# Kernel optimization log

Measured on AMD Instinct MI355X. Metric: run time of the kernel, lower is better.

Reference implementation:

```python
import jax, jax.numpy as jnp
import numpy as np

N_NODES = 50000
N_EDGES = 800000
NUM_MOL = 2000
MSG_PASSES = 4


def setup_inputs() -> dict:
    key = jax.random.key(0)
    ks = jax.random.split(key, 16)
    x = jax.random.randint(ks[0], (N_NODES,), 0, 119)
    edge_attr = jax.random.randint(ks[1], (N_EDGES,), 0, 4)
    edge_index = jax.random.randint(ks[2], (2, N_EDGES), 0, N_NODES)
    batch = jnp.sort(jax.random.randint(ks[3], (N_NODES,), 0, NUM_MOL))
    f32 = jnp.float32
    return {
        "x": x,
        "edge_attr": edge_attr,
        "edge_index": edge_index,
        "batch": batch,
        "atom_table": jax.random.normal(ks[4], (119, 128), f32) * 0.1,
        "bond_table": jax.random.normal(ks[5], (4, 64), f32) * 0.1,
        "Wi": jax.random.normal(ks[6], (192, 128), f32) * 0.05,
        "bi": jax.random.normal(ks[7], (128,), f32) * 0.01,
        "Wu1": jax.random.normal(ks[8], (320, 128), f32) * 0.05,
        "bu1": jax.random.normal(ks[9], (128,), f32) * 0.01,
        "Wu2": jax.random.normal(ks[10], (128, 128), f32) * 0.05,
        "bu2": jax.random.normal(ks[11], (128,), f32) * 0.01,
        "Wr1": jax.random.normal(ks[12], (128, 512), f32) * 0.05,
        "br1": jax.random.normal(ks[13], (512,), f32) * 0.01,
        "Wr2": jax.random.normal(ks[14], (512, 1), f32) * 0.05,
        "br2": jax.random.normal(ks[15], (1,), f32) * 0.01,
    }


def reference(x, edge_attr, edge_index, batch,
              atom_table, bond_table, Wi, bi, Wu1, bu1, Wu2, bu2,
              Wr1, br1, Wr2, br2):
    atom = atom_table[x]                      # [N, atom_emb]
    bond = bond_table[edge_attr]              # [E, bond_emb]
    src, dst = edge_index[0], edge_index[1]
    a_src = atom[src]                         # [E, atom_emb]
    ab = jnp.concatenate([a_src, bond], axis=1)  # [E, atom_emb+bond_emb]
    msg = jax.nn.relu(ab @ Wi + bi)           # [E, msg_dim]
    for _ in range(MSG_PASSES):
        agg = jax.ops.segment_sum(msg, dst, num_segments=N_NODES)  # [N, msg_dim]
        upd_in = jnp.concatenate([ab, agg[src]], axis=1)           # [E, 320]
        h = jax.nn.relu(upd_in @ Wu1 + bu1)
        msg = jax.nn.relu(h @ Wu2 + bu2)
    node_state = jax.ops.segment_sum(msg, dst, num_segments=N_NODES)
    mol_state = jax.ops.segment_sum(node_state, batch, num_segments=NUM_MOL)
    out = jax.nn.relu(mol_state @ Wr1 + br1) @ Wr2 + br2  # [NUM_MOL, 1]
    return jnp.squeeze(out, axis=-1)
```

## Files before the change

kernel.cpp:

```cpp
#include <hip/hip_runtime.h>
#include <hip/hip_bf16.h>

#define N_NODES 50000
#define N_EDGES 800000
#define NUM_MOL 2000

typedef __attribute__((ext_vector_type(8))) short short8;
typedef __attribute__((ext_vector_type(4))) float f32x4;

union bfbits { __hip_bfloat16 b; short s; };

__global__ void k_tables(const float* __restrict__ atom_table,
                         const float* __restrict__ bond_table,
                         const float* __restrict__ Wi,
                         const float* __restrict__ bi,
                         const float* __restrict__ Wu1,
                         const float* __restrict__ bu1,
                         float* __restrict__ T1, float* __restrict__ U1,
                         float* __restrict__ T2c, float* __restrict__ U2c) {
  int b = blockIdx.x;
  int c = threadIdx.x;
  if (b < 119) {
    float t = 0.f, u = 0.f;
    for (int k = 0; k < 128; k++) {
      float a = atom_table[b * 128 + k];
      t += a * Wi[k * 128 + c];
      u += a * Wu1[k * 128 + c];
    }
    T1[b * 128 + c] = t;
    U1[b * 128 + c] = u;
  } else {
    int a = b - 119;
    float t = bi[c], u = bu1[c];
    for (int k = 0; k < 64; k++) {
      float bv = bond_table[a * 64 + k];
      t += bv * Wi[(128 + k) * 128 + c];
      u += bv * Wu1[(128 + k) * 128 + c];
    }
    T2c[a * 128 + c] = t;
    U2c[a * 128 + c] = u;
  }
}

__global__ void k_prep(const float* __restrict__ T1, const float* __restrict__ T2c,
                       const float* __restrict__ Wu2, const float* __restrict__ Wu1,
                       float* __restrict__ TT,
                       short* __restrict__ Wt, short* __restrict__ Wlo,
                       short* __restrict__ W1t, short* __restrict__ W1lo) {
  int b = blockIdx.x;
  int k = threadIdx.x;
  if (b < 476) {
    float v = T1[(b >> 2) * 128 + k] + T2c[(b & 3) * 128 + k];
    TT[b * 128 + k] = v > 0.f ? v : 0.f;
  } else if (b < 604) {
    int n = b - 476;
    float w = Wu2[k * 128 + n];
    bfbits hi; hi.b = __float2bfloat16(w);
    float hf = __bfloat162float(hi.b);
    bfbits lo; lo.b = __float2bfloat16(w - hf);
    Wt[n * 128 + k] = hi.s;
    Wlo[n * 128 + k] = lo.s;
  } else {
    int n = b - 604;
    float w = Wu1[(192 + k) * 128 + n];
    bfbits hi; hi.b = __float2bfloat16(w);
    float hf = __bfloat162float(hi.b);
    bfbits lo; lo.b = __float2bfloat16(w - hf);
    W1t[n * 128 + k] = hi.s;
    W1lo[n * 128 + k] = lo.s;
  }
}

__global__ void k_fillb(const int* __restrict__ eidx, const int* __restrict__ attr,
                        const int* __restrict__ x,
                        int* __restrict__ cnt, int* __restrict__ csr1) {
  int e = blockIdx.x * 256 + threadIdx.x;
  int d = eidx[N_EDGES + e];
  int s = eidx[e];
  int a = attr[e];
  int pos = atomicAdd(&cnt[d], 1);
  if (pos < 64) {
    int packed = (s * 4 + a) | ((x[s] * 4 + a) << 18);
    csr1[d * 64 + pos] = packed;
  }
}

__global__ void k_molptr(const int* __restrict__ batch, int* __restrict__ molptr) {
  int m = blockIdx.x * 256 + threadIdx.x;
  if (m > NUM_MOL) return;
  int lo = 0, hi = N_NODES;
  while (lo < hi) {
    int mid = (lo + hi) >> 1;
    if (batch[mid] < m) lo = mid + 1; else hi = mid;
  }
  molptr[m] = lo;
}

__global__ void k_gather0(const int* __restrict__ cnt, const int* __restrict__ csr1,
                          const float* __restrict__ TT, float* __restrict__ A_) {
  int n = blockIdx.x * 4 + (threadIdx.x >> 6);
  int lane = threadIdx.x & 63;
  int g = lane >> 5;
  int p = lane & 31;
  int beg = n * 64;
  int end = beg + cnt[n];
  float s0 = 0.f, s1 = 0.f, s2 = 0.f, s3 = 0.f;
  int i = beg;
  for (; i + 7 < end; i += 8) {
    int iA = ((unsigned)csr1[i + g]) >> 18;
    int iB = ((unsigned)csr1[i + 2 + g]) >> 18;
    int iC = ((unsigned)csr1[i + 4 + g]) >> 18;
    int iD = ((unsigned)csr1[i + 6 + g]) >> 18;
    float4 va = *(const float4*)&TT[iA * 128 + p * 4];
    float4 vb = *(const float4*)&TT[iB * 128 + p * 4];
    float4 vc = *(const float4*)&TT[iC * 128 + p * 4];
    float4 vd = *(const float4*)&TT[iD * 128 + p * 4];
    s0 += (va.x + vb.x) + (vc.x + vd.x);
    s1 += (va.y + vb.y) + (vc.y + vd.y);
    s2 += (va.z + vb.z) + (vc.z + vd.z);
    s3 += (va.w + vb.w) + (vc.w + vd.w);
  }
  for (; i + 3 < end; i += 4) {
    int iA = ((unsigned)csr1[i + g]) >> 18;
    int iB = ((unsigned)csr1[i + 2 + g]) >> 18;
    float4 va = *(const float4*)&TT[iA * 128 + p * 4];
    float4 vb = *(const float4*)&TT[iB * 128 + p * 4];
    s0 += va.x + vb.x; s1 += va.y + vb.y;
    s2 += va.z + vb.z; s3 += va.w + vb.w;
  }
  for (; i < end; i += 2) {
    if (i + g < end) {
      int idx = ((unsigned)csr1[i + g]) >> 18;
      float4 v = *(const float4*)&TT[idx * 128 + p * 4];
      s0 += v.x; s1 += v.y; s2 += v.z; s3 += v.w;
    }
  }
  s0 += __shfl_xor(s0, 32, 64);
  s1 += __shfl_xor(s1, 32, 64);
  s2 += __shfl_xor(s2, 32, 64);
  s3 += __shfl_xor(s3, 32, 64);
  float2 o;
  o.x = (g == 0) ? s0 : s2;
  o.y = (g == 0) ? s1 : s3;
  *(float2*)&A_[n * 128 + p * 4 + g * 2] = o;
}

__global__ void k_gather(const int* __restrict__ cnt, const int* __restrict__ csr1,
                         const __hip_bfloat16* __restrict__ M, float* __restrict__ A_) {
  int n = blockIdx.x * 4 + (threadIdx.x >> 6);
  int lane = threadIdx.x & 63;
  int g = lane >> 4;
  int p = lane & 15;
  int beg = n * 64;
  int end = beg + cnt[n];
  float s[8];
#pragma unroll
  for (int j = 0; j < 8; j++) s[j] = 0.f;
  const short* Ms = (const short*)M;
  int i = beg;
  for (; i + 15 < end; i += 16) {
    int iA = csr1[i + g] & 0x3FFFF;
    int iB = csr1[i + 4 + g] & 0x3FFFF;
    int iC = csr1[i + 8 + g] & 0x3FFFF;
    int iD = csr1[i + 12 + g] & 0x3FFFF;
    short8 va = *(const short8*)&Ms[iA * 128 + p * 8];
    short8 vb = *(const short8*)&Ms[iB * 128 + p * 8];
    short8 vc = *(const short8*)&Ms[iC * 128 + p * 8];
    short8 vd = *(const short8*)&Ms[iD * 128 + p * 8];
#pragma unroll
    for (int j = 0; j < 4; j++) {
      float2 fa = __bfloat1622float2(*(const __hip_bfloat162*)&((const short*)&va)[j * 2]);
      float2 fb = __bfloat1622float2(*(const __hip_bfloat162*)&((const short*)&vb)[j * 2]);
      float2 fc = __bfloat1622float2(*(const __hip_bfloat162*)&((const short*)&vc)[j * 2]);
      float2 fd = __bfloat1622float2(*(const __hip_bfloat162*)&((const short*)&vd)[j * 2]);
      s[j * 2] += (fa.x + fb.x) + (fc.x + fd.x);
      s[j * 2 + 1] += (fa.y + fb.y) + (fc.y + fd.y);
    }
  }
  for (; i + 7 < end; i += 8) {
    int iA = csr1[i + g] & 0x3FFFF;
    int iB = csr1[i + 4 + g] & 0x3FFFF;
    short8 va = *(const short8*)&Ms[iA * 128 + p * 8];
    short8 vb = *(const short8*)&Ms[iB * 128 + p * 8];
#pragma unroll
    for (int j = 0; j < 4; j++) {
      float2 fa = __bfloat1622float2(*(const __hip_bfloat162*)&((const short*)&va)[j * 2]);
      float2 fb = __bfloat1622float2(*(const __hip_bfloat162*)&((const short*)&vb)[j * 2]);
      s[j * 2] += fa.x + fb.x;
      s[j * 2 + 1] += fa.y + fb.y;
    }
  }
  for (; i < end; i += 4) {
    if (i + g < end) {
      int idx = csr1[i + g] & 0x3FFFF;
      short8 va = *(const short8*)&Ms[idx * 128 + p * 8];
#pragma unroll
      for (int j = 0; j < 4; j++) {
        float2 fa = __bfloat1622float2(*(const __hip_bfloat162*)&((const short*)&va)[j * 2]);
        s[j * 2] += fa.x;
        s[j * 2 + 1] += fa.y;
      }
    }
  }
#pragma unroll
  for (int j = 0; j < 8; j++) s[j] += __shfl_xor(s[j], 16, 64);
#pragma unroll
  for (int j = 0; j < 8; j++) s[j] += __shfl_xor(s[j], 32, 64);
  float2 o;
  o.x = s[g * 2];
  o.y = s[g * 2 + 1];
  *(float2*)&A_[n * 128 + p * 8 + g * 2] = o;
}

__global__ __launch_bounds__(256, 2) void k_mm1m(const float* __restrict__ A_,
                                                 const short* __restrict__ W1t,
                                                 const short* __restrict__ W1lo,
                                                 const int* __restrict__ x,
                                                 const float* __restrict__ U1,
                                                 float* __restrict__ B2_) {
  __shared__ short wh[8192];
  __shared__ short wl[8192];
  __shared__ float mbuf[4][16][68];
  int t = threadIdx.x;
  int lane = t & 63;
  int m = lane & 15;
  int quad = lane >> 4;
  int wslot = t >> 6;
  int h = blockIdx.x & 1;

  for (int idx = t; idx < 1024; idx += 256) {
    int nl = idx >> 4;
    int c16 = idx & 15;
    int off = nl * 256 + c16 * 16;
    int so = (off ^ ((nl & 7) << 4)) >> 1;
    *(short8*)&wh[so] = *(const short8*)((const char*)W1t + (h * 64 + nl) * 256 + c16 * 16);
    *(short8*)&wl[so] = *(const short8*)((const char*)W1lo + (h * 64 + nl) * 256 + c16 * 16);
  }
  int nb[4], nx[4];
#pragma unroll
  for (int nt = 0; nt < 4; nt++) {
    int nl = nt * 16 + m;
    nb[nt] = nl * 256;
    nx[nt] = (nl & 7) << 4;
  }
  __syncthreads();

  for (int s = (blockIdx.x >> 1) * 4 + wslot; s < 3125; s += 2048) {
    int row = s * 16 + m;
    f32x4 acc[4];
#pragma unroll
    for (int nt = 0; nt < 4; nt++) acc[nt] = (f32x4){0.f, 0.f, 0.f, 0.f};

#pragma unroll
    for (int kc = 0; kc < 4; kc++) {
      int k0 = kc * 32 + quad * 8;
      short8 ahi, alo;
      {
        float av[8];
        *(float4*)&av[0] = *(const float4*)&A_[row * 128 + k0];
        *(float4*)&av[4] = *(const float4*)&A_[row * 128 + k0 + 4];
#pragma unroll
        for (int j = 0; j < 8; j++) {
          float hv = av[j];
          bfbits hi; hi.b = __float2bfloat16(hv);
          float hf = __bfloat162float(hi.b);
          bfbits lo; lo.b = __float2bfloat16(hv - hf);
          ahi[j] = hi.s;
          alo[j] = lo.s;
        }
      }
      int kb = k0 * 2;
#pragma unroll
      for (int nt = 0; nt < 4; nt++) {
        int so = ((nb[nt] + kb) ^ nx[nt]) >> 1;
        short8 whv = *(const short8*)&wh[so];
        short8 wlv = *(const short8*)&wl[so];
        acc[nt] = __builtin_amdgcn_mfma_f32_16x16x32_bf16(ahi, whv, acc[nt], 0, 0, 0);
        acc[nt] = __builtin_amdgcn_mfma_f32_16x16x32_bf16(alo, whv, acc[nt], 0, 0, 0);
        acc[nt] = __builtin_amdgcn_mfma_f32_16x16x32_bf16(ahi, wlv, acc[nt], 0, 0, 0);
      }
    }

#pragma unroll
    for (int nt = 0; nt < 4; nt++)
#pragma unroll
      for (int r = 0; r < 4; r++)
        mbuf[wslot][quad * 4 + r][nt * 16 + m] = acc[nt][r];
#pragma unroll
    for (int p = 0; p < 4; p++) {
      int c = p * 64 + lane;
      int rr = c >> 4;
      int qf = c & 15;
      int n = s * 16 + rr;
      int xn = x[n];
      float4 v = *(const float4*)&mbuf[wslot][rr][qf * 4];
      float4 d = *(const float4*)&U1[xn * 128 + h * 64 + qf * 4];
      v.x += d.x; v.y += d.y; v.z += d.z; v.w += d.w;
      *(float4*)&B2_[n * 128 + h * 64 + qf * 4] = v;
    }
  }
}

__global__ __launch_bounds__(256, 2) void k_mm2(const float* __restrict__ B2_,
                                                const float* __restrict__ U2c,
                                                const short* __restrict__ Wt,
                                                const short* __restrict__ Wlo,
                                                const float* __restrict__ bu2,
                                                __hip_bfloat16* __restrict__ M) {
  __shared__ short wh[16384];
  __shared__ short wl[16384];
  __shared__ short mbuf[4][16][68];
  int t = threadIdx.x;
  int lane = t & 63;
  int m = lane & 15;
  int quad = lane >> 4;
  int wslot = t >> 6;
  int w0 = blockIdx.x * 4 + wslot;
  int h = w0 & 1;

  for (int idx = t; idx < 2048; idx += 256) {
    int n = idx >> 4;
    int c16 = idx & 15;
    int off = n * 256 + c16 * 16;
    int so = (off ^ ((n & 7) << 4)) >> 1;
    *(short8*)&wh[so] = *(const short8*)((const char*)Wt + off);
    *(short8*)&wl[so] = *(const short8*)((const char*)Wlo + off);
  }
  float bias[4];
  int nb[4], nx[4];
#pragma unroll
  for (int nt = 0; nt < 4; nt++) {
    int n = h * 64 + nt * 16 + m;
    bias[nt] = bu2[n];
    nb[nt] = n * 256;
    nx[nt] = (n & 7) << 4;
  }
  __syncthreads();

  for (int tid = w0; tid < 25000; tid += 4096) {
    int s = tid >> 1;
    int node = s * 4 + (m >> 2);
    int attr = m & 3;
    f32x4 acc[4];
#pragma unroll
    for (int nt = 0; nt < 4; nt++) acc[nt] = (f32x4){0.f, 0.f, 0.f, 0.f};

#pragma unroll
    for (int kc = 0; kc < 4; kc++) {
      int k0 = kc * 32 + quad * 8;
      short8 ahi, alo;
      {
        float bba[8], u2a[8];
        *(float4*)&bba[0] = *(const float4*)&B2_[node * 128 + k0];
        *(float4*)&bba[4] = *(const float4*)&B2_[node * 128 + k0 + 4];
        *(float4*)&u2a[0] = *(const float4*)&U2c[attr * 128 + k0];
        *(float4*)&u2a[4] = *(const float4*)&U2c[attr * 128 + k0 + 4];
#pragma unroll
        for (int j = 0; j < 8; j++) {
          float hv = bba[j] + u2a[j];
          hv = hv > 0.f ? hv : 0.f;
          bfbits hi; hi.b = __float2bfloat16(hv);
          float hf = __bfloat162float(hi.b);
          bfbits lo; lo.b = __float2bfloat16(hv - hf);
          ahi[j] = hi.s;
          alo[j] = lo.s;
        }
      }
      int kb = k0 * 2;
#pragma unroll
      for (int nt = 0; nt < 4; nt++) {
        int so = ((nb[nt] + kb) ^ nx[nt]) >> 1;
        short8 whv = *(const short8*)&wh[so];
        short8 wlv = *(const short8*)&wl[so];
        acc[nt] = __builtin_amdgcn_mfma_f32_16x16x32_bf16(ahi, whv, acc[nt], 0, 0, 0);
        acc[nt] = __builtin_amdgcn_mfma_f32_16x16x32_bf16(alo, whv, acc[nt], 0, 0, 0);
        acc[nt] = __builtin_amdgcn_mfma_f32_16x16x32_bf16(ahi, wlv, acc[nt], 0, 0, 0);
      }
    }

#pragma unroll
    for (int nt = 0; nt < 4; nt++) {
#pragma unroll
      for (int r = 0; r < 4; r++) {
        float v = acc[nt][r] + bias[nt];
        v = v > 0.f ? v : 0.f;
        bfbits o; o.b = __float2bfloat16(v);
        mbuf[wslot][quad * 4 + r][nt * 16 + m] = o.s;
      }
    }
    {
      int rr = lane >> 2;
      int qq = lane & 3;
      short8 v = *(const short8*)&mbuf[wslot][rr][qq * 8];
      *(short8*)((short*)M + (s * 16 + rr) * 128 + h * 64 + qq * 8) = v;
      short8 v2 = *(const short8*)&mbuf[wslot][rr][(qq + 4) * 8];
      *(short8*)((short*)M + (s * 16 + rr) * 128 + h * 64 + (qq + 4) * 8) = v2;
    }
  }
}

__global__ void k_molgather(const float* __restrict__ A_, const int* __restrict__ molptr,
                            float* __restrict__ mol) {
  int m = blockIdx.x * 4 + (threadIdx.x >> 6);
  int lane = threadIdx.x & 63;
  int beg = molptr[m], end = molptr[m + 1];
  float ax = 0.f, ay = 0.f;
  int n = beg;
  for (; n + 1 < end; n += 2) {
    float2 v0 = *(const float2*)&A_[n * 128 + lane * 2];
    float2 v1 = *(const float2*)&A_[(n + 1) * 128 + lane * 2];
    ax += v0.x + v1.x;
    ay += v0.y + v1.y;
  }
  if (n < end) {
    float2 v0 = *(const float2*)&A_[n * 128 + lane * 2];
    ax += v0.x;
    ay += v0.y;
  }
  float2 o; o.x = ax; o.y = ay;
  *(float2*)&mol[m * 128 + lane * 2] = o;
}

__global__ __launch_bounds__(256) void k_readout(const float* __restrict__ mol,
                                                 const float* __restrict__ Wr1,
                                                 const float* __restrict__ br1,
                                                 const float* __restrict__ Wr2,
                                                 const float* __restrict__ br2,
                                                 float* __restrict__ out) {
  int m0 = blockIdx.x * 8;
  __shared__ float ms[8][128];
  __shared__ float red[32];
  int t = threadIdx.x;
  int lane = t & 63;
  int wave = t >> 6;
  for (int i = t; i < 1024; i += 256)
    ms[i >> 7][i & 127] = mol[m0 * 128 + i];
  __syncthreads();
  float part[8];
#pragma unroll
  for (int q = 0; q < 8; q++) part[q] = 0.f;
#pragma unroll
  for (int jj = 0; jj < 2; jj++) {
    int j = t + jj * 256;
    float b1 = br1[j];
    float acc[8];
#pragma unroll
    for (int q = 0; q < 8; q++) acc[q] = b1;
    for (int k = 0; k < 128; k += 4) {
      float w0 = Wr1[k * 512 + j];
      float w1 = Wr1[(k + 1) * 512 + j];
      float w2 = Wr1[(k + 2) * 512 + j];
      float w3 = Wr1[(k + 3) * 512 + j];
#pragma unroll
      for (int q = 0; q < 8; q++)
        acc[q] += ms[q][k] * w0 + ms[q][k + 1] * w1 + ms[q][k + 2] * w2 + ms[q][k + 3] * w3;
    }
    float w2v = Wr2[j];
#pragma unroll
    for (int q = 0; q < 8; q++) {
      float a = acc[q] > 0.f ? acc[q] : 0.f;
      part[q] += a * w2v;
    }
  }
#pragma unroll
  for (int q = 0; q < 8; q++) {
    float v = part[q];
    v += __shfl_xor(v, 32, 64);
    v += __shfl_xor(v, 16, 64);
    v += __shfl_xor(v, 8, 64);
    v += __shfl_xor(v, 4, 64);
    v += __shfl_xor(v, 2, 64);
    v += __shfl_xor(v, 1, 64);
    if (lane == 0) red[wave * 8 + q] = v;
  }
  __syncthreads();
  if (t < 8)
    out[m0 + t] = red[t] + red[8 + t] + red[16 + t] + red[24 + t] + br2[0];
}

extern "C" void kernel_launch(void* const* d_in, const int* in_sizes, int n_in,
                              void* d_out, int out_size, void* d_ws, size_t ws_size,
                              hipStream_t stream) {
  const int* x        = (const int*)d_in[0];
  const int* eattr    = (const int*)d_in[1];
  const int* eidx     = (const int*)d_in[2];
  const int* batch    = (const int*)d_in[3];
  const float* atom_table = (const float*)d_in[4];
  const float* bond_table = (const float*)d_in[5];
  const float* Wi  = (const float*)d_in[6];
  const float* bi  = (const float*)d_in[7];
  const float* Wu1 = (const float*)d_in[8];
  const float* bu1 = (const float*)d_in[9];
  const float* Wu2 = (const float*)d_in[10];
  const float* bu2 = (const float*)d_in[11];
  const float* Wr1 = (const float*)d_in[12];
  const float* br1 = (const float*)d_in[13];
  const float* Wr2 = (const float*)d_in[14];
  const float* br2 = (const float*)d_in[15];
  float* out = (float*)d_out;

  char* ws = (char*)d_ws;
  __hip_bfloat16* M = (__hip_bfloat16*)(ws);
  short* Wt      = (short*)(ws + 51200000);
  short* Wlo     = (short*)(ws + 51232768);
  short* W1t     = (short*)(ws + 51265536);
  short* W1lo    = (short*)(ws + 51298304);
  int*   molptr  = (int*)  (ws + 51331072);
  int*   cnt     = (int*)  (ws + 51340000);
  int*   csr1    = (int*)  (ws + 52000000);
  float* A       = (float*)(ws + 102400000);
  float* B2      = (float*)(ws + 128000000);
  float* T1      = (float*)(ws + 157000064);
  float* U1      = (float*)(ws + 157060992);
  float* T2c     = (float*)(ws + 157121920);
  float* U2c     = (float*)(ws + 157123968);
  float* TT      = (float*)(ws + 157126016);
  float* mol     = (float*)(ws + 157369728);

  hipMemsetAsync(cnt, 0, N_NODES * sizeof(int), stream);
  k_tables<<<123, 128, 0, stream>>>(atom_table, bond_table, Wi, bi, Wu1, bu1,
                                    T1, U1, T2c, U2c);
  k_prep<<<732, 128, 0, stream>>>(T1, T2c, Wu2, Wu1, TT, Wt, Wlo, W1t, W1lo);
  k_fillb<<<N_EDGES / 256, 256, 0, stream>>>(eidx, eattr, x, cnt, csr1);
  k_molptr<<<(NUM_MOL + 256) / 256, 256, 0, stream>>>(batch, molptr);

  k_gather0<<<N_NODES / 4, 256, 0, stream>>>(cnt, csr1, TT, A);

  for (int p = 0; p < 4; p++) {
    k_mm1m<<<1024, 256, 0, stream>>>(A, W1t, W1lo, x, U1, B2);
    k_mm2<<<1024, 256, 0, stream>>>(B2, U2c, Wt, Wlo, bu2, M);
    k_gather<<<N_NODES / 4, 256, 0, stream>>>(cnt, csr1, M, A);
  }

  k_molgather<<<NUM_MOL / 4, 256, 0, stream>>>(A, molptr, mol);
  k_readout<<<NUM_MOL / 8, 256, 0, stream>>>(mol, Wr1, br1, Wr2, br2, out);
}
```

Baseline: 547.1 us.

## Restructure k_mm2 so each block holds one weight half and loops over bond attrs

Each block now loads only its half of the second-layer weights into shared memory, which halves LDS per block. Each wave processes 16 nodes and loops over all 4 bond attributes, reusing one B2 row load across four (node, attr) rows instead of reloading per attribute. The output row mapping changes to (node*4+attr). This quadruples the accumulator registers (16 f32x4 per lane), which may reduce occupancy.

After: 767.0 us. 1.4x slower.

```diff
diff --git a/kernel.cpp b/kernel.cpp
--- a/kernel.cpp
+++ b/kernel.cpp
@@ -307,54 +307,56 @@
                                                 const short* __restrict__ Wlo,
                                                 const float* __restrict__ bu2,
                                                 __hip_bfloat16* __restrict__ M) {
-  __shared__ short wh[16384];
-  __shared__ short wl[16384];
+  __shared__ short wh[8192];
+  __shared__ short wl[8192];
   __shared__ short mbuf[4][16][68];
   int t = threadIdx.x;
   int lane = t & 63;
   int m = lane & 15;
   int quad = lane >> 4;
   int wslot = t >> 6;
-  int w0 = blockIdx.x * 4 + wslot;
-  int h = w0 & 1;
-
-  for (int idx = t; idx < 2048; idx += 256) {
-    int n = idx >> 4;
+  int h = blockIdx.x & 1;
+
+  for (int idx = t; idx < 1024; idx += 256) {
+    int nl = idx >> 4;
     int c16 = idx & 15;
-    int off = n * 256 + c16 * 16;
-    int so = (off ^ ((n & 7) << 4)) >> 1;
-    *(short8*)&wh[so] = *(const short8*)((const char*)Wt + off);
-    *(short8*)&wl[so] = *(const short8*)((const char*)Wlo + off);
+    int off = nl * 256 + c16 * 16;
+    int so = (off ^ ((nl & 7) << 4)) >> 1;
+    *(short8*)&wh[so] = *(const short8*)((const char*)Wt + (h * 64 + nl) * 256 + c16 * 16);
+    *(short8*)&wl[so] = *(const short8*)((const char*)Wlo + (h * 64 + nl) * 256 + c16 * 16);
   }
   float bias[4];
   int nb[4], nx[4];
 #pragma unroll
   for (int nt = 0; nt < 4; nt++) {
-    int n = h * 64 + nt * 16 + m;
-    bias[nt] = bu2[n];
-    nb[nt] = n * 256;
-    nx[nt] = (n & 7) << 4;
+    int nl = nt * 16 + m;
+    bias[nt] = bu2[h * 64 + nl];
+    nb[nt] = nl * 256;
+    nx[nt] = (nl & 7) << 4;
   }
   __syncthreads();
 
-  for (int tid = w0; tid < 25000; tid += 4096) {
-    int s = tid >> 1;
-    int node = s * 4 + (m >> 2);
-    int attr = m & 3;
-    f32x4 acc[4];
-#pragma unroll
-    for (int nt = 0; nt < 4; nt++) acc[nt] = (f32x4){0.f, 0.f, 0.f, 0.f};
+  for (int s = (blockIdx.x >> 1) * 4 + wslot; s < 3125; s += 2048) {
+    int row = s * 16 + m;
+    f32x4 acc[4][4];
+#pragma unroll
+    for (int a = 0; a < 4; a++)
+#pragma unroll
+      for (int nt = 0; nt < 4; nt++) acc[a][nt] = (f32x4){0.f, 0.f, 0.f, 0.f};
 
 #pragma unroll
     for (int kc = 0; kc < 4; kc++) {
       int k0 = kc * 32 + quad * 8;
-      short8 ahi, alo;
-      {
-        float bba[8], u2a[8];
-        *(float4*)&bba[0] = *(const float4*)&B2_[node * 128 + k0];
-        *(float4*)&bba[4] = *(const float4*)&B2_[node * 128 + k0 + 4];
-        *(float4*)&u2a[0] = *(const float4*)&U2c[attr * 128 + k0];
-        *(float4*)&u2a[4] = *(const float4*)&U2c[attr * 128 + k0 + 4];
+      float bba[8];
+      *(float4*)&bba[0] = *(const float4*)&B2_[row * 128 + k0];
+      *(float4*)&bba[4] = *(const float4*)&B2_[row * 128 + k0 + 4];
+      int kb = k0 * 2;
+#pragma unroll
+      for (int a = 0; a < 4; a++) {
+        float u2a[8];
+        *(float4*)&u2a[0] = *(const float4*)&U2c[a * 128 + k0];
+        *(float4*)&u2a[4] = *(const float4*)&U2c[a * 128 + k0 + 4];
+        short8 ahi, alo;
 #pragma unroll
         for (int j = 0; j < 8; j++) {
           float hv = bba[j] + u2a[j];
@@ -365,36 +367,39 @@
           ahi[j] = hi.s;
           alo[j] = lo.s;
         }
+#pragma unroll
+        for (int nt = 0; nt < 4; nt++) {
+          int so = ((nb[nt] + kb) ^ nx[nt]) >> 1;
+          short8 whv = *(const short8*)&wh[so];
+          short8 wlv = *(const short8*)&wl[so];
+          acc[a][nt] = __builtin_amdgcn_mfma_f32_16x16x32_bf16(ahi, whv, acc[a][nt], 0, 0, 0);
+          acc[a][nt] = __builtin_amdgcn_mfma_f32_16x16x32_bf16(alo, whv, acc[a][nt], 0, 0, 0);
+          acc[a][nt] = __builtin_amdgcn_mfma_f32_16x16x32_bf16(ahi, wlv, acc[a][nt], 0, 0, 0);
+        }
       }
-      int kb = k0 * 2;
+    }
+
+#pragma unroll
+    for (int a = 0; a < 4; a++) {
 #pragma unroll
       for (int nt = 0; nt < 4; nt++) {
-        int so = ((nb[nt] + kb) ^ nx[nt]) >> 1;
-        short8 whv = *(const short8*)&wh[so];
-        short8 wlv = *(const short8*)&wl[so];
-        acc[nt] = __builtin_amdgcn_mfma_f32_16x16x32_bf16(ahi, whv, acc[nt], 0, 0, 0);
-        acc[nt] = __builtin_amdgcn_mfma_f32_16x16x32_bf16(alo, whv, acc[nt], 0, 0, 0);
-        acc[nt] = __builtin_amdgcn_mfma_f32_16x16x32_bf16(ahi, wlv, acc[nt], 0, 0, 0);
+#pragma unroll
+        for (int r = 0; r < 4; r++) {
+          float v = acc[a][nt][r] + bias[nt];
+          v = v > 0.f ? v : 0.f;
+          bfbits o; o.b = __float2bfloat16(v);
+          mbuf[wslot][quad * 4 + r][nt * 16 + m] = o.s;
+        }
       }
-    }
-
-#pragma unroll
-    for (int nt = 0; nt < 4; nt++) {
-#pragma unroll
-      for (int r = 0; r < 4; r++) {
-        float v = acc[nt][r] + bias[nt];
-        v = v > 0.f ? v : 0.f;
-        bfbits o; o.b = __float2bfloat16(v);
-        mbuf[wslot][quad * 4 + r][nt * 16 + m] = o.s;
+      {
+        int rr = lane >> 2;
+        int qq = lane & 3;
+        int mrow = (s * 16 + rr) * 4 + a;
+        short8 v = *(const short8*)&mbuf[wslot][rr][qq * 8];
+        *(short8*)((short*)M + mrow * 128 + h * 64 + qq * 8) = v;
+        short8 v2 = *(const short8*)&mbuf[wslot][rr][(qq + 4) * 8];
+        *(short8*)((short*)M + mrow * 128 + h * 64 + (qq + 4) * 8) = v2;
       }
-    }
-    {
-      int rr = lane >> 2;
-      int qq = lane & 3;
-      short8 v = *(const short8*)&mbuf[wslot][rr][qq * 8];
-      *(short8*)((short*)M + (s * 16 + rr) * 128 + h * 64 + qq * 8) = v;
-      short8 v2 = *(const short8*)&mbuf[wslot][rr][(qq + 4) * 8];
-      *(short8*)((short*)M + (s * 16 + rr) * 128 + h * 64 + (qq + 4) * 8) = v2;
     }
   }
 }
```
